# Performance work log

Hardware: AMD Instinct MI355X
Metric: run time of the kernel (lower is better)

Reference implementation:

```python
import jax, jax.numpy as jnp
import numpy as np
import math

B, NRES, RPR = 1, 384, 3
L = NRES * RPR          # 1152 rigids
CS, CZ = 256, 128
CH, H, PQ, PV = 16, 8, 8, 12


def _ln(x, scale, bias):
    mu = jnp.mean(x, axis=-1, keepdims=True)
    var = jnp.var(x, axis=-1, keepdims=True)
    return (x - mu) * jax.lax.rsqrt(var + 1e-5) * scale + bias


def _quat_to_rot(q):
    q = q / jnp.linalg.norm(q, axis=-1, keepdims=True)
    w, x, y, z = q[..., 0], q[..., 1], q[..., 2], q[..., 3]
    r = jnp.stack([
        1 - 2 * (y * y + z * z), 2 * (x * y - w * z), 2 * (x * z + w * y),
        2 * (x * y + w * z), 1 - 2 * (x * x + z * z), 2 * (y * z - w * x),
        2 * (x * z - w * y), 2 * (y * z + w * x), 1 - 2 * (x * x + y * y),
    ], axis=-1)
    return r.reshape(q.shape[:-1] + (3, 3))


def setup_inputs() -> dict:
    key = jax.random.key(0)
    ks = jax.random.split(key, 20)
    s = jax.random.normal(ks[0], (B, L, CS), jnp.float32)
    z = jax.random.normal(ks[1], (B, NRES, NRES, CZ), jnp.float32)
    rot = _quat_to_rot(jax.random.normal(ks[2], (B, L, 4), jnp.float32))
    trans = 10.0 * jax.random.normal(ks[3], (B, L, 3), jnp.float32)
    mask = jnp.ones((B, L), jnp.float32)
    rigid_to_res_idx = jnp.broadcast_to(jnp.arange(L, dtype=jnp.int32) // RPR, (B, L))
    w = lambda k, sh: 0.02 * jax.random.normal(k, sh, jnp.float32)
    return {
        "s": s, "z": z, "rot": rot, "trans": trans, "mask": mask,
        "ln_s_scale": jnp.ones((CS,), jnp.float32), "ln_s_bias": jnp.zeros((CS,), jnp.float32),
        "ln_z_scale": jnp.ones((CZ,), jnp.float32), "ln_z_bias": jnp.zeros((CZ,), jnp.float32),
        "w_q": w(ks[4], (CS, H * CH)), "w_k": w(ks[5], (CS, H * CH)), "w_v": w(ks[6], (CS, H * CH)),
        "w_qp": w(ks[7], (CS, H * PQ * 3)), "w_kp": w(ks[8], (CS, H * PQ * 3)), "w_vp": w(ks[9], (CS, H * PV * 3)),
        "w_b": w(ks[10], (CZ, H)),
        "head_weights": jnp.full((H,), 0.5413, jnp.float32),  # softplus^-1(1)
        "w_out": w(ks[11], (H * (CH + CZ + PV * 4), CS)),
        "b_out": jnp.zeros((CS,), jnp.float32),
        "rigid_to_res_idx": rigid_to_res_idx,
    }


def reference(s, z, rot, trans, mask, ln_s_scale, ln_s_bias, ln_z_scale, ln_z_bias,
              w_q, w_k, w_v, w_qp, w_kp, w_vp, w_b, head_weights, w_out, b_out,
              rigid_to_res_idx):
    b_, l_ = s.shape[0], s.shape[1]
    idx = rigid_to_res_idx[0]                       # [L] rigid -> residue, shared over batch
    s_ln = _ln(s, ln_s_scale, ln_s_bias)            # [B,L,CS]
    z_ln = _ln(z, ln_z_scale, ln_z_bias)            # [B,N,N,CZ]

    q = (s_ln @ w_q).reshape(b_, l_, H, CH)
    k = (s_ln @ w_k).reshape(b_, l_, H, CH)
    v = (s_ln @ w_v).reshape(b_, l_, H, CH)

    # local points, then rigid-transform to global frame: x_g = R x + t
    q_p = (s_ln @ w_qp).reshape(b_, l_, H, PQ, 3)
    k_p = (s_ln @ w_kp).reshape(b_, l_, H, PQ, 3)
    v_p = (s_ln @ w_vp).reshape(b_, l_, H, PV, 3)
    t5 = trans[:, :, None, None, :]
    q_g = jnp.einsum("blij,blhpj->blhpi", rot, q_p) + t5
    k_g = jnp.einsum("blij,blhpj->blhpi", rot, k_p) + t5
    v_g = jnp.einsum("blij,blhpj->blhpi", rot, v_p) + t5

    # scalar qk term
    a = jnp.einsum("blhc,bjhc->bhlj", q, k) * math.sqrt(1.0 / (3 * CH))
    # pair bias, broadcast residue-pair -> rigid-pair
    b_res = z_ln @ w_b                                # [B,N,N,H]
    b_full = b_res[:, idx][:, :, idx]                 # [B,L,L,H]
    a = a + math.sqrt(1.0 / 3) * jnp.transpose(b_full, (0, 3, 1, 2))
    # point-distance term: ||q-k||^2 = |q|^2 + |k|^2 - 2 q.k (summed over P,3)
    hw = jax.nn.softplus(head_weights) * math.sqrt(1.0 / (3 * (PQ * 9.0 / 2)))
    qq = jnp.sum(q_g * q_g, axis=(-1, -2)).transpose(0, 2, 1)   # [B,H,L]
    kk = jnp.sum(k_g * k_g, axis=(-1, -2)).transpose(0, 2, 1)
    qk = jnp.einsum("blhpc,bjhpc->bhlj", q_g, k_g)
    d2 = qq[:, :, :, None] + kk[:, :, None, :] - 2.0 * qk
    a = a - 0.5 * d2 * hw[None, :, None, None]
    a = a + (mask[:, None, None, :] - 1.0) * 1e9
    attn = jax.nn.softmax(a, axis=-1)                 # [B,H,L,L]

    o = jnp.einsum("bhlj,bjhc->blhc", attn, v)        # [B,L,H,CH]
    o_pt_g = jnp.einsum("bhlj,bjhpc->blhpc", attn, v_g)
    # back to local frame of query rigid: R^T (x - t)
    o_pt = jnp.einsum("blji,blhpj->blhpi", rot, o_pt_g - t5)
    o_pt_norm = jnp.sqrt(jnp.sum(o_pt * o_pt, axis=-1) + 1e-8)  # [B,L,H,PV]
    # pair output: sum attention over rigids belonging to each key residue
    attn_res = attn.reshape(b_, H, l_, NRES, RPR).sum(-1)       # [B,H,L,N]
    z_l = z_ln[:, idx]                                           # [B,L,N,CZ]
    o_pair = jnp.einsum("bhln,blnc->blhc", attn_res, z_l)        # [B,L,H,CZ]

    cat = jnp.concatenate(
        [o, o_pt.reshape(b_, l_, H, PV * 3), o_pt_norm, o_pair], axis=-1
    ).reshape(b_, l_, H * (CH + PV * 4 + CZ))
    return cat @ w_out + b_out                        # [B,L,CS]
```

## Files before the change

### kernel.cpp

```cpp
#include <hip/hip_runtime.h>
#include <hip/hip_bf16.h>

#define L 1152
#define NRES 384
#define CS 256
#define CZ 128
#define H 8
#define CH 16
#define PQ 8
#define PV 12
#define PSTR 1088

#define OFF_SLN  0L
#define OFF_PROJ 294912L
#define OFF_WPK  1548288L
#define OFF_QCAT 1826816L
#define OFF_KCAT 2232320L
#define OFF_VCAT 2637824L
#define OFF_BRES 3227648L
#define OFF_MURS 4407296L
#define OFF_ATTN 4702208L
#define OFF_CAT  15319040L
#define OFF_PCAT 17088512L

__global__ __launch_bounds__(256) void k_ln_s(const float* s, const float* sc, const float* bi, float* sln){
  int l = blockIdx.x, t = threadIdx.x;
  __shared__ float red[CS];
  float x = s[(long)l*CS + t];
  red[t] = x; __syncthreads();
  for(int st=128; st>0; st>>=1){ if(t<st) red[t]+=red[t+st]; __syncthreads(); }
  float mu = red[0] * (1.f/CS); __syncthreads();
  float d = x - mu;
  red[t] = d*d; __syncthreads();
  for(int st=128; st>0; st>>=1){ if(t<st) red[t]+=red[t+st]; __syncthreads(); }
  float var = red[0]*(1.f/CS);
  sln[(long)l*CS + t] = d*rsqrtf(var + 1e-5f)*sc[t] + bi[t];
}

__global__ __launch_bounds__(256) void k_packw(const float* wq, const float* wk, const float* wv,
                        const float* wqp, const float* wkp, const float* wvp, float* wpack){
  int k = blockIdx.x, t = threadIdx.x;
  for(int c=t; c<PSTR; c+=256){
    float v;
    if(c<128)        v = wq [(long)k*128 + c];
    else if(c<256)   v = wk [(long)k*128 + c-128];
    else if(c<384)   v = wv [(long)k*128 + c-256];
    else if(c<576)   v = wqp[(long)k*192 + c-384];
    else if(c<768)   v = wkp[(long)k*192 + c-576];
    else if(c<1056)  v = wvp[(long)k*288 + c-768];
    else             v = 0.f;
    wpack[(long)k*PSTR + c] = v;
  }
}

__global__ __launch_bounds__(256) void k_proj(const float* sln, const float* wpack, float* proj){
  int l0 = blockIdx.x*64, c0 = blockIdx.y*64, t = threadIdx.x;
  __shared__ float a_s[32][68];
  __shared__ __align__(16) float w_s[32][68];
  int tr = t>>4, tc = t&15;
  float4 acc[4] = {{0,0,0,0},{0,0,0,0},{0,0,0,0},{0,0,0,0}};
  for(int kc=0; kc<8; kc++){
    int k0 = kc*32;
    {
      int row = t>>2, kk0 = (t&3)*8;
      const float4* src = (const float4*)(sln + (long)(l0+row)*256 + k0 + kk0);
      float4 v0 = src[0], v1 = src[1];
      a_s[kk0+0][row]=v0.x; a_s[kk0+1][row]=v0.y; a_s[kk0+2][row]=v0.z; a_s[kk0+3][row]=v0.w;
      a_s[kk0+4][row]=v1.x; a_s[kk0+5][row]=v1.y; a_s[kk0+6][row]=v1.z; a_s[kk0+7][row]=v1.w;
    }
    #pragma unroll
    for(int kk2=0; kk2<2; kk2++){
      int kk = (t>>4) + 16*kk2;
      *(float4*)&w_s[kk][(t&15)*4] = *(const float4*)(wpack + (long)(k0+kk)*PSTR + c0 + (t&15)*4);
    }
    __syncthreads();
    #pragma unroll 8
    for(int kk=0; kk<32; kk++){
      float4 a4 = *(const float4*)&a_s[kk][tr*4];
      float4 b4 = *(const float4*)&w_s[kk][tc*4];
      acc[0].x+=a4.x*b4.x; acc[0].y+=a4.x*b4.y; acc[0].z+=a4.x*b4.z; acc[0].w+=a4.x*b4.w;
      acc[1].x+=a4.y*b4.x; acc[1].y+=a4.y*b4.y; acc[1].z+=a4.y*b4.z; acc[1].w+=a4.y*b4.w;
      acc[2].x+=a4.z*b4.x; acc[2].y+=a4.z*b4.y; acc[2].z+=a4.z*b4.z; acc[2].w+=a4.z*b4.w;
      acc[3].x+=a4.w*b4.x; acc[3].y+=a4.w*b4.y; acc[3].z+=a4.w*b4.z; acc[3].w+=a4.w*b4.w;
    }
    __syncthreads();
  }
  #pragma unroll
  for(int r=0;r<4;r++)
    *(float4*)(proj + (long)(l0 + tr*4 + r)*PSTR + c0 + tc*4) = acc[r];
}

__global__ __launch_bounds__(256) void k_ln_z(const float* z, const float* sc, const float* bi,
                       const float* wb, float* murs, float* bres_t){
  int t = threadIdx.x;
  long rp0 = (long)blockIdx.x*32;
  int r = t>>3, part = t&7;
  long rp = rp0 + r;
  __shared__ __align__(16) float swb[8*132];
  __shared__ float SB[8][2];
  const float4* z4 = (const float4*)z;
  float4 x0 = z4[rp*32 + part*4 + 0];
  float4 x1 = z4[rp*32 + part*4 + 1];
  float4 x2 = z4[rp*32 + part*4 + 2];
  float4 x3 = z4[rp*32 + part*4 + 3];
  #pragma unroll
  for(int k2=0;k2<4;k2++){
    int e = t + k2*256; int h = e>>7, c = e&127;
    swb[h*132 + c] = sc[c]*wb[(long)c*8 + h];
  }
  __syncthreads();
  if(t < 64){
    int h = t>>3, seg = t&7;
    float S=0, Bv=0;
    #pragma unroll
    for(int i=0;i<16;i++){
      int c = seg*16+i;
      S  += swb[h*132+c];
      Bv += bi[c]*wb[(long)c*8 + h];
    }
    #pragma unroll
    for(int off=1;off<8;off<<=1){ S += __shfl_xor(S,off,64); Bv += __shfl_xor(Bv,off,64); }
    if(seg==0){ SB[h][0]=S; SB[h][1]=Bv; }
  }
  float s1 = x0.x+x0.y+x0.z+x0.w + x1.x+x1.y+x1.z+x1.w
           + x2.x+x2.y+x2.z+x2.w + x3.x+x3.y+x3.z+x3.w;
  float s2 = x0.x*x0.x+x0.y*x0.y+x0.z*x0.z+x0.w*x0.w
           + x1.x*x1.x+x1.y*x1.y+x1.z*x1.z+x1.w*x1.w
           + x2.x*x2.x+x2.y*x2.y+x2.z*x2.z+x2.w*x2.w
           + x3.x*x3.x+x3.y*x3.y+x3.z*x3.z+x3.w*x3.w;
  #pragma unroll
  for(int off=1;off<8;off<<=1){ s1 += __shfl_xor(s1,off,64); s2 += __shfl_xor(s2,off,64); }
  float mu = s1*(1.f/CZ);
  float var = s2*(1.f/CZ) - mu*mu;
  float rstd = rsqrtf(var + 1e-5f);
  if(part==0){ murs[rp*2]=mu; murs[rp*2+1]=rstd; }
  float acc[8];
  const float4* swb4 = (const float4*)swb;
  #pragma unroll
  for(int h=0;h<8;h++){
    float4 wa = swb4[h*33 + part*4 + 0];
    float4 wbv= swb4[h*33 + part*4 + 1];
    float4 wc = swb4[h*33 + part*4 + 2];
    float4 wd = swb4[h*33 + part*4 + 3];
    acc[h] = x0.x*wa.x + x0.y*wa.y + x0.z*wa.z + x0.w*wa.w
           + x1.x*wbv.x+ x1.y*wbv.y+ x1.z*wbv.z+ x1.w*wbv.w
           + x2.x*wc.x + x2.y*wc.y + x2.z*wc.z + x2.w*wc.w
           + x3.x*wd.x + x3.y*wd.y + x3.z*wd.z + x3.w*wd.w;
  }
  #pragma unroll
  for(int off=1;off<8;off<<=1){
    #pragma unroll
    for(int h=0;h<8;h++) acc[h] += __shfl_xor(acc[h],off,64);
  }
  __syncthreads();
  if(part==0){
    #pragma unroll
    for(int h=0;h<8;h++)
      bres_t[(long)h*147456 + rp] = rstd*(acc[h] - mu*SB[h][0]) + SB[h][1];
  }
}

__global__ __launch_bounds__(256) void k_rigid(const float* proj, const float* rot, const float* trans,
                        const float* mask, const float* hws,
                        float* qcat, float* kcat, float* vcat){
  int l = blockIdx.x, t = threadIdx.x;
  __shared__ float R[9], T[3], hwS[8], qgs[192], kgs[192];
  if(t<9) R[t]=rot[(long)l*9+t];
  if(t<3) T[t]=trans[(long)l*3+t];
  if(t>=16 && t<24) hwS[t-16] = log1pf(expf(hws[t-16]))*0.09622504486493764f;
  __syncthreads();
  const float* pr = proj + (long)l*PSTR;
  if(t<128){
    int h=t>>4, c=t&15;
    long base = ((long)h*L + l)*44;
    qcat[base + c] = 0.14433756729740643f * pr[t];
    kcat[base + c] = pr[128+t];
    vcat[((long)h*L + l)*64 + c] = pr[256+t];
  }
  if(t < 192){
    int h=t/24, m=t%24, p=m/3, i=m%3;
    float qa = R[i*3+0]*pr[384+h*24+p*3+0] + R[i*3+1]*pr[384+h*24+p*3+1]
             + R[i*3+2]*pr[384+h*24+p*3+2] + T[i];
    float ka = R[i*3+0]*pr[576+h*24+p*3+0] + R[i*3+1]*pr[576+h*24+p*3+1]
             + R[i*3+2]*pr[576+h*24+p*3+2] + T[i];
    qgs[t]=qa; kgs[t]=ka;
    long base = ((long)h*L + l)*44 + 16 + m;
    qcat[base] = hwS[h]*qa;
    kcat[base] = ka;
  }
  for(int it=t; it<288; it+=256){
    int h=it/36, m=it%36, p=m/3, i=m%3;
    float a = R[i*3+0]*pr[768+h*36+p*3+0] + R[i*3+1]*pr[768+h*36+p*3+1]
            + R[i*3+2]*pr[768+h*36+p*3+2] + T[i];
    vcat[((long)h*L + l)*64 + 16 + m] = a;
  }
  if(t < 96){
    int h=t/12, d=t%12;
    vcat[((long)h*L + l)*64 + 52 + d] = 0.f;
  }
  __syncthreads();
  if(t < 8){
    float qq=0, kk=0;
    #pragma unroll
    for(int m=0;m<24;m++){ qq += qgs[t*24+m]*qgs[t*24+m]; kk += kgs[t*24+m]*kgs[t*24+m]; }
    long base = ((long)t*L + l)*44;
    qcat[base + 40] = -0.5f*hwS[t]*qq;
    kcat[base + 40] = -0.5f*hwS[t]*kk + (mask[l]-1.f)*1e9f;
  }
}

__global__ __launch_bounds__(256) void k_scores(const float* qcat, const float* kcat,
                         const float* bres_t, const int* ridx, float* attn){
  int l0 = blockIdx.x*32, j0 = blockIdx.y*64, h = blockIdx.z;
  int t = threadIdx.x;
  __shared__ __align__(16) float q_s[32*44];
  __shared__ __align__(16) float k_s[64*44];
  __shared__ int rj_s[64];
  {
    const float* srcq = qcat + ((long)h*L + l0)*44;
    for(int i=t; i<32*44; i+=256) q_s[i]=srcq[i];
    const float* srck = kcat + ((long)h*L + j0)*44;
    for(int i=t; i<64*44; i+=256) k_s[i]=srck[i];
    if(t<64) rj_s[t]=ridx[j0+t];
  }
  __syncthreads();
  int a = t>>5;
  int b = t&31;
  float acc[4][2] = {{0,0},{0,0},{0,0},{0,0}};
  const float4* q4 = (const float4*)q_s;
  const float4* k4 = (const float4*)k_s;
  #pragma unroll
  for(int i=0;i<10;i++){
    float4 kA = k4[(long)b*11 + i];
    float4 kB = k4[(long)(b+32)*11 + i];
    #pragma unroll
    for(int r=0;r<4;r++){
      float4 qv = q4[(long)(a+8*r)*11 + i];
      acc[r][0] += qv.x*kA.x + qv.y*kA.y + qv.z*kA.z + qv.w*kA.w;
      acc[r][1] += qv.x*kB.x + qv.y*kB.y + qv.z*kB.z + qv.w*kB.w;
    }
  }
  float colc0 = k_s[b*44+40], colc1 = k_s[(b+32)*44+40];
  int rj0 = rj_s[b], rj1 = rj_s[b+32];
  const float* bbh = bres_t + (long)h*147456;
  #pragma unroll
  for(int r=0;r<4;r++){
    int row = a+8*r;
    float rowc = q_s[row*44+40];
    int rl = ridx[l0+row];
    const float* bb = bbh + (long)rl*NRES;
    float s0 = acc[r][0] + rowc + colc0 + 0.5773502691896258f*bb[rj0];
    float s1 = acc[r][1] + rowc + colc1 + 0.5773502691896258f*bb[rj1];
    float* arow = attn + ((long)h*L + l0+row)*L + j0;
    arow[b]    = s0;
    arow[b+32] = s1;
  }
}

__global__ __launch_bounds__(256) void k_smax(float* attn){
  long row = (long)blockIdx.x*4 + (threadIdx.x>>6);
  int lane = threadIdx.x & 63;
  float* p = attn + row*L;
  float v[18];
  float m=-1e30f;
  #pragma unroll
  for(int i=0;i<18;i++){ v[i]=p[lane + i*64]; m=fmaxf(m,v[i]); }
  #pragma unroll
  for(int off=1;off<64;off<<=1) m=fmaxf(m,__shfl_xor(m,off,64));
  float s=0;
  #pragma unroll
  for(int i=0;i<18;i++){ v[i]=__expf(v[i]-m); s+=v[i]; }
  #pragma unroll
  for(int off=1;off<64;off<<=1) s+=__shfl_xor(s,off,64);
  float inv=1.f/s;
  #pragma unroll
  for(int i=0;i<18;i++) p[lane+i*64]=v[i]*inv;
}

__global__ __launch_bounds__(256) void k_av(const float* attn, const float* vcat,
                     const float* rot, const float* trans, float* cat){
  int lb = blockIdx.x, h = blockIdx.y, t = threadIdx.x;
  int l0 = lb*32;
  __shared__ float a_s[64][33];
  __shared__ __align__(16) float v_s[64][68];
  __shared__ __align__(16) float fin_s[32][64];
  int lgrp = t>>4, dgrp = t&15;
  float4 acc0 = {0,0,0,0}, acc1 = {0,0,0,0};
  const float* abase = attn + ((long)h*L + l0)*L;
  for(int jc=0; jc<18; jc++){
    int j0 = jc*64;
    {
      int al = t>>3, jj0 = (t&7)*8;
      const float4* src = (const float4*)(abase + (long)al*L + j0 + jj0);
      float4 p0 = src[0], p1 = src[1];
      a_s[jj0+0][al]=p0.x; a_s[jj0+1][al]=p0.y; a_s[jj0+2][al]=p0.z; a_s[jj0+3][al]=p0.w;
      a_s[jj0+4][al]=p1.x; a_s[jj0+5][al]=p1.y; a_s[jj0+6][al]=p1.z; a_s[jj0+7][al]=p1.w;
    }
    {
      int jj = t>>2, seg = t&3;
      const float4* src = (const float4*)(vcat + ((long)h*L + j0 + jj)*64 + seg*16);
      float4 q0=src[0], q1=src[1], q2=src[2], q3=src[3];
      float4* dst = (float4*)&v_s[jj][seg*16];
      dst[0]=q0; dst[1]=q1; dst[2]=q2; dst[3]=q3;
    }
    __syncthreads();
    #pragma unroll 8
    for(int jj=0; jj<64; jj++){
      float a0 = a_s[jj][lgrp*2], a1 = a_s[jj][lgrp*2+1];
      const float4 vv = *(const float4*)&v_s[jj][dgrp*4];
      acc0.x+=a0*vv.x; acc0.y+=a0*vv.y; acc0.z+=a0*vv.z; acc0.w+=a0*vv.w;
      acc1.x+=a1*vv.x; acc1.y+=a1*vv.y; acc1.z+=a1*vv.z; acc1.w+=a1*vv.w;
    }
    __syncthreads();
  }
  *(float4*)&fin_s[lgrp*2+0][dgrp*4] = acc0;
  *(float4*)&fin_s[lgrp*2+1][dgrp*4] = acc1;
  __syncthreads();
  for(int it=t; it<32*16; it+=256){
    int l=it>>4, c=it&15;
    cat[(long)(l0+l)*1536 + h*192 + c] = fin_s[l][c];
  }
  for(int it=t; it<32*12; it+=256){
    int l=it/12, p=it%12;
    long gl = l0+l;
    float og0 = fin_s[l][16+p*3+0]-trans[gl*3+0];
    float og1 = fin_s[l][16+p*3+1]-trans[gl*3+1];
    float og2 = fin_s[l][16+p*3+2]-trans[gl*3+2];
    float* crow = cat + gl*1536 + h*192;
    float nrm=0;
    #pragma unroll
    for(int i=0;i<3;i++){
      float v = rot[gl*9+0+i]*og0 + rot[gl*9+3+i]*og1 + rot[gl*9+6+i]*og2;
      crow[16+p*3+i]=v; nrm+=v*v;
    }
    crow[52+p]=sqrtf(nrm+1e-8f);
  }
}

__global__ __launch_bounds__(256) void k_opair(const float* attn, const float* z, const float* murs,
                        const float* sc, const float* bi, const int* ridx, float* cat){
  int r=blockIdx.x, t=threadIdx.x;
  __shared__ __align__(16) float ar[3][H][NRES];
  __shared__ __align__(16) float mrs[NRES*2];
  int rl = ridx[r*3];
  for(int it=t; it<3*H*NRES; it+=256){
    int lo = it/(H*NRES);
    int rem = it - lo*(H*NRES);
    int h = rem/NRES, n = rem - h*NRES;
    const float* arow = attn + ((long)h*L + r*3+lo)*L + n*3;
    ar[lo][h][n]=arow[0]+arow[1]+arow[2];
  }
  for(int i=t;i<NRES*2;i+=256) mrs[i]=murs[(long)rl*NRES*2 + i];
  __syncthreads();
  int tc=t&63, th=t>>6;
  int c0=tc*2, h0=th*2;
  float sc0=sc[c0], sc1=sc[c0+1], bi0=bi[c0], bi1=bi[c0+1];
  float acc[3][2][2]={};
  const float* zbase = z + ((long)rl*NRES)*CZ + c0;
  for(int n=0;n<NRES;n+=2){
    float4 mr4 = *(const float4*)&mrs[n*2];
    float2 z0 = *(const float2*)(zbase + (long)n*CZ);
    float2 z1 = *(const float2*)(zbase + (long)(n+1)*CZ);
    float zv00 = (z0.x - mr4.x)*mr4.y*sc0 + bi0;
    float zv01 = (z0.y - mr4.x)*mr4.y*sc1 + bi1;
    float zv10 = (z1.x - mr4.z)*mr4.w*sc0 + bi0;
    float zv11 = (z1.y - mr4.z)*mr4.w*sc1 + bi1;
    #pragma unroll
    for(int lo=0;lo<3;lo++){
      #pragma unroll
      for(int hp=0;hp<2;hp++){
        float2 a2 = *(const float2*)&ar[lo][h0+hp][n];
        acc[lo][hp][0] += a2.x*zv00 + a2.y*zv10;
        acc[lo][hp][1] += a2.x*zv01 + a2.y*zv11;
      }
    }
  }
  #pragma unroll
  for(int lo=0;lo<3;lo++){
    float* crow = cat + (long)(r*3+lo)*1536;
    #pragma unroll
    for(int hp=0;hp<2;hp++){
      crow[(h0+hp)*192+64+c0]   = acc[lo][hp][0];
      crow[(h0+hp)*192+64+c0+1] = acc[lo][hp][1];
    }
  }
}

__global__ __launch_bounds__(256) void k_final(const float* cat, const float* wout, float* pcat){
  int l0 = blockIdx.x*32, c0 = blockIdx.y*32, kp = blockIdx.z, t = threadIdx.x;
  __shared__ float a_s[64][33];
  __shared__ __align__(16) float w_s[64][36];
  int tr = t>>3, tc = t&7;
  float4 acc = {0,0,0,0};
  for(int kc=0; kc<6; kc++){
    int k0 = kp*384 + kc*64;
    {
      int row = t>>3, kk0 = (t&7)*8;
      const float4* src = (const float4*)(cat + (long)(l0+row)*1536 + k0 + kk0);
      float4 v0 = src[0], v1 = src[1];
      a_s[kk0+0][row]=v0.x; a_s[kk0+1][row]=v0.y; a_s[kk0+2][row]=v0.z; a_s[kk0+3][row]=v0.w;
      a_s[kk0+4][row]=v1.x; a_s[kk0+5][row]=v1.y; a_s[kk0+6][row]=v1.z; a_s[kk0+7][row]=v1.w;
    }
    #pragma unroll
    for(int kk2=0; kk2<2; kk2++){
      int kk = (t>>3) + 32*kk2;
      *(float4*)&w_s[kk][(t&7)*4] = *(const float4*)(wout + (long)(k0+kk)*256 + c0 + (t&7)*4);
    }
    __syncthreads();
    #pragma unroll 8
    for(int kk=0; kk<64; kk++){
      float a0 = a_s[kk][tr];
      float4 b4 = *(const float4*)&w_s[kk][tc*4];
      acc.x+=a0*b4.x; acc.y+=a0*b4.y; acc.z+=a0*b4.z; acc.w+=a0*b4.w;
    }
    __syncthreads();
  }
  *(float4*)(pcat + ((long)kp*L + l0+tr)*256 + c0 + tc*4) = acc;
}

__global__ __launch_bounds__(256) void k_redout(const float* pcat, const float* bout, float* out){
  int i = blockIdx.x*256 + threadIdx.x;
  const float4* p = (const float4*)pcat;
  float4 a = p[i], b = p[i+73728], c = p[i+147456], d = p[i+221184];
  float4 bv = ((const float4*)bout)[i&63];
  float4 r;
  r.x = a.x+b.x+c.x+d.x+bv.x;
  r.y = a.y+b.y+c.y+d.y+bv.y;
  r.z = a.z+b.z+c.z+d.z+bv.z;
  r.w = a.w+b.w+c.w+d.w+bv.w;
  ((float4*)out)[i] = r;
}

extern "C" void kernel_launch(void* const* d_in, const int* in_sizes, int n_in,
                              void* d_out, int out_size, void* d_ws, size_t ws_size,
                              hipStream_t stream) {
  const float* s      = (const float*)d_in[0];
  const float* z      = (const float*)d_in[1];
  const float* rot    = (const float*)d_in[2];
  const float* trans  = (const float*)d_in[3];
  const float* mask   = (const float*)d_in[4];
  const float* lnss   = (const float*)d_in[5];
  const float* lnsb   = (const float*)d_in[6];
  const float* lnzs   = (const float*)d_in[7];
  const float* lnzb   = (const float*)d_in[8];
  const float* wq     = (const float*)d_in[9];
  const float* wk     = (const float*)d_in[10];
  const float* wv     = (const float*)d_in[11];
  const float* wqp    = (const float*)d_in[12];
  const float* wkp    = (const float*)d_in[13];
  const float* wvp    = (const float*)d_in[14];
  const float* wb     = (const float*)d_in[15];
  const float* hws    = (const float*)d_in[16];
  const float* wout   = (const float*)d_in[17];
  const float* bout   = (const float*)d_in[18];
  const int*  ridx    = (const int*)d_in[19];

  float* ws  = (float*)d_ws;
  float* out = (float*)d_out;

  float* sln  = ws + OFF_SLN;
  float* proj = ws + OFF_PROJ;
  float* wpk  = ws + OFF_WPK;
  float* qcat = ws + OFF_QCAT;
  float* kcat = ws + OFF_KCAT;
  float* vcat = ws + OFF_VCAT;
  float* bres = ws + OFF_BRES;
  float* murs = ws + OFF_MURS;
  float* attn = ws + OFF_ATTN;
  float* cat  = ws + OFF_CAT;
  float* pcat = ws + OFF_PCAT;

  k_packw<<<dim3(256), dim3(256), 0, stream>>>(wq, wk, wv, wqp, wkp, wvp, wpk);
  k_ln_s<<<dim3(L), dim3(CS), 0, stream>>>(s, lnss, lnsb, sln);
  k_proj<<<dim3(18,17), dim3(256), 0, stream>>>(sln, wpk, proj);
  k_ln_z<<<dim3(NRES*NRES/32), dim3(256), 0, stream>>>(z, lnzs, lnzb, wb, murs, bres);
  k_rigid<<<dim3(L), dim3(256), 0, stream>>>(proj, rot, trans, mask, hws, qcat, kcat, vcat);
  k_scores<<<dim3(L/32, L/64, H), dim3(256), 0, stream>>>(qcat, kcat, bres, ridx, attn);
  k_smax<<<dim3(H*L/4), dim3(256), 0, stream>>>(attn);
  k_av<<<dim3(L/32, H), dim3(256), 0, stream>>>(attn, vcat, rot, trans, cat);
  k_opair<<<dim3(NRES), dim3(256), 0, stream>>>(attn, z, murs, lnzs, lnzb, ridx, cat);
  k_final<<<dim3(36,8,4), dim3(256), 0, stream>>>(cat, wout, pcat);
  k_redout<<<dim3(288), dim3(256), 0, stream>>>(pcat, bout, out);
}
```

Measured before the change: 356.3 us.

## Defer softmax normalization into consumers and split AV over key chunks

Replaces the in-place softmax with a row-stat kernel that stores only the max and inverse sum per row. The AV and pair-output kernels recompute the exponentials on load, which removes the full write-back of the attention matrix. The AV kernel is also split three ways along the key dimension to get more blocks, with a new reduction kernel that sums the partials and does the frame transform. In exchange, exponentials are computed twice, there is an extra launch, and the partial buffer reuses the workspace region at offset zero.

```diff
diff --git a/kernel.cpp b/kernel.cpp
--- a/kernel.cpp
+++ b/kernel.cpp
@@ -22,6 +22,8 @@
 #define OFF_ATTN 4702208L
 #define OFF_CAT  15319040L
 #define OFF_PCAT 17088512L
+#define OFF_RSTAT 18268160L
+#define OFF_PAV  0L
 
 __global__ __launch_bounds__(256) void k_ln_s(const float* s, const float* sc, const float* bi, float* sln){
   int l = blockIdx.x, t = threadIdx.x;
@@ -257,10 +259,10 @@
   }
 }
 
-__global__ __launch_bounds__(256) void k_smax(float* attn){
+__global__ __launch_bounds__(256) void k_rowstat(const float* attn, float* rowstat){
   long row = (long)blockIdx.x*4 + (threadIdx.x>>6);
   int lane = threadIdx.x & 63;
-  float* p = attn + row*L;
+  const float* p = attn + row*L;
   float v[18];
   float m=-1e30f;
   #pragma unroll
@@ -269,32 +271,37 @@
   for(int off=1;off<64;off<<=1) m=fmaxf(m,__shfl_xor(m,off,64));
   float s=0;
   #pragma unroll
-  for(int i=0;i<18;i++){ v[i]=__expf(v[i]-m); s+=v[i]; }
+  for(int i=0;i<18;i++) s+=__expf(v[i]-m);
   #pragma unroll
   for(int off=1;off<64;off<<=1) s+=__shfl_xor(s,off,64);
-  float inv=1.f/s;
-  #pragma unroll
-  for(int i=0;i<18;i++) p[lane+i*64]=v[i]*inv;
+  if(lane==0){ rowstat[row*2]=m; rowstat[row*2+1]=1.f/s; }
 }
 
 __global__ __launch_bounds__(256) void k_av(const float* attn, const float* vcat,
-                     const float* rot, const float* trans, float* cat){
-  int lb = blockIdx.x, h = blockIdx.y, t = threadIdx.x;
+                     const float* rowstat, float* pav){
+  int lb = blockIdx.x, h = blockIdx.y, sp = blockIdx.z, t = threadIdx.x;
   int l0 = lb*32;
   __shared__ float a_s[64][33];
   __shared__ __align__(16) float v_s[64][68];
-  __shared__ __align__(16) float fin_s[32][64];
   int lgrp = t>>4, dgrp = t&15;
   float4 acc0 = {0,0,0,0}, acc1 = {0,0,0,0};
   const float* abase = attn + ((long)h*L + l0)*L;
-  for(int jc=0; jc<18; jc++){
+  int al = t>>3, jj0 = (t&7)*8;
+  float mrow = rowstat[((long)h*L + l0 + al)*2];
+  float irow = rowstat[((long)h*L + l0 + al)*2 + 1];
+  for(int jc=sp*6; jc<sp*6+6; jc++){
     int j0 = jc*64;
     {
-      int al = t>>3, jj0 = (t&7)*8;
       const float4* src = (const float4*)(abase + (long)al*L + j0 + jj0);
       float4 p0 = src[0], p1 = src[1];
-      a_s[jj0+0][al]=p0.x; a_s[jj0+1][al]=p0.y; a_s[jj0+2][al]=p0.z; a_s[jj0+3][al]=p0.w;
-      a_s[jj0+4][al]=p1.x; a_s[jj0+5][al]=p1.y; a_s[jj0+6][al]=p1.z; a_s[jj0+7][al]=p1.w;
+      a_s[jj0+0][al]=__expf(p0.x-mrow)*irow;
+      a_s[jj0+1][al]=__expf(p0.y-mrow)*irow;
+      a_s[jj0+2][al]=__expf(p0.z-mrow)*irow;
+      a_s[jj0+3][al]=__expf(p0.w-mrow)*irow;
+      a_s[jj0+4][al]=__expf(p1.x-mrow)*irow;
+      a_s[jj0+5][al]=__expf(p1.y-mrow)*irow;
+      a_s[jj0+6][al]=__expf(p1.z-mrow)*irow;
+      a_s[jj0+7][al]=__expf(p1.w-mrow)*irow;
     }
     {
       int jj = t>>2, seg = t&3;
@@ -313,8 +320,27 @@
     }
     __syncthreads();
   }
-  *(float4*)&fin_s[lgrp*2+0][dgrp*4] = acc0;
-  *(float4*)&fin_s[lgrp*2+1][dgrp*4] = acc1;
+  float* dst = pav + (((long)sp*H + h)*L + l0 + lgrp*2)*64 + dgrp*4;
+  *(float4*)dst = acc0;
+  *(float4*)(dst + 64) = acc1;
+}
+
+__global__ __launch_bounds__(256) void k_avred(const float* pav, const float* rot, const float* trans,
+                        float* cat){
+  int lb = blockIdx.x, h = blockIdx.y, t = threadIdx.x;
+  int l0 = lb*32;
+  __shared__ __align__(16) float fin_s[32][64];
+  #pragma unroll
+  for(int k=0;k<2;k++){
+    int fi = t + k*256;
+    int l = fi>>4, c4 = fi&15;
+    long base = (((long)h)*L + l0 + l)*64 + c4*4;
+    float4 a = *(const float4*)(pav + base);
+    float4 b = *(const float4*)(pav + 589824 + base);
+    float4 c = *(const float4*)(pav + 1179648 + base);
+    float4 r = {a.x+b.x+c.x, a.y+b.y+c.y, a.z+b.z+c.z, a.w+b.w+c.w};
+    *(float4*)&fin_s[l][c4*4] = r;
+  }
   __syncthreads();
   for(int it=t; it<32*16; it+=256){
     int l=it>>4, c=it&15;
@@ -338,17 +364,26 @@
 }
 
 __global__ __launch_bounds__(256) void k_opair(const float* attn, const float* z, const float* murs,
+                        const float* rowstat,
                         const float* sc, const float* bi, const int* ridx, float* cat){
   int r=blockIdx.x, t=threadIdx.x;
   __shared__ __align__(16) float ar[3][H][NRES];
   __shared__ __align__(16) float mrs[NRES*2];
+  __shared__ float rs_s[24][2];
   int rl = ridx[r*3];
+  if(t<24){
+    int lo=t/8, h=t%8;
+    long row = (long)h*L + r*3+lo;
+    rs_s[t][0]=rowstat[row*2]; rs_s[t][1]=rowstat[row*2+1];
+  }
+  __syncthreads();
   for(int it=t; it<3*H*NRES; it+=256){
     int lo = it/(H*NRES);
     int rem = it - lo*(H*NRES);
     int h = rem/NRES, n = rem - h*NRES;
     const float* arow = attn + ((long)h*L + r*3+lo)*L + n*3;
-    ar[lo][h][n]=arow[0]+arow[1]+arow[2];
+    float m = rs_s[lo*8+h][0], iv = rs_s[lo*8+h][1];
+    ar[lo][h][n]=(__expf(arow[0]-m)+__expf(arow[1]-m)+__expf(arow[2]-m))*iv;
   }
   for(int i=t;i<NRES*2;i+=256) mrs[i]=murs[(long)rl*NRES*2 + i];
   __syncthreads();
@@ -469,6 +504,8 @@
   float* attn = ws + OFF_ATTN;
   float* cat  = ws + OFF_CAT;
   float* pcat = ws + OFF_PCAT;
+  float* rstat= ws + OFF_RSTAT;
+  float* pav  = ws + OFF_PAV;
 
   k_packw<<<dim3(256), dim3(256), 0, stream>>>(wq, wk, wv, wqp, wkp, wvp, wpk);
   k_ln_s<<<dim3(L), dim3(CS), 0, stream>>>(s, lnss, lnsb, sln);
@@ -476,9 +513,10 @@
   k_ln_z<<<dim3(NRES*NRES/32), dim3(256), 0, stream>>>(z, lnzs, lnzb, wb, murs, bres);
   k_rigid<<<dim3(L), dim3(256), 0, stream>>>(proj, rot, trans, mask, hws, qcat, kcat, vcat);
   k_scores<<<dim3(L/32, L/64, H), dim3(256), 0, stream>>>(qcat, kcat, bres, ridx, attn);
-  k_smax<<<dim3(H*L/4), dim3(256), 0, stream>>>(attn);
-  k_av<<<dim3(L/32, H), dim3(256), 0, stream>>>(attn, vcat, rot, trans, cat);
-  k_opair<<<dim3(NRES), dim3(256), 0, stream>>>(attn, z, murs, lnzs, lnzb, ridx, cat);
+  k_rowstat<<<dim3(H*L/4), dim3(256), 0, stream>>>(attn, rstat);
+  k_av<<<dim3(L/32, H, 3), dim3(256), 0, stream>>>(attn, vcat, rstat, pav);
+  k_avred<<<dim3(L/32, H), dim3(256), 0, stream>>>(pav, rot, trans, cat);
+  k_opair<<<dim3(NRES), dim3(256), 0, stream>>>(attn, z, murs, rstat, lnzs, lnzb, ridx, cat);
   k_final<<<dim3(36,8,4), dim3(256), 0, stream>>>(cat, wout, pcat);
   k_redout<<<dim3(288), dim3(256), 0, stream>>>(pcat, bout, out);
 }
```

New measurement: 338.8 us. 4.9% less time.
